# Performance work log

Hardware: AMD Instinct MI355X
Metric: run time of the kernel (lower is better)

The kernel has to match this reference:

```python
import jax, jax.numpy as jnp
import numpy as np
import math

DIM = 32
CODEBOOK_SIZE = 16384
LOG_N = int(math.log(CODEBOOK_SIZE, 2))  # 14
LOGVAR_MIN, LOGVAR_MAX = -30.0, 20.0
TOL = 0.5
BETA = 1.0
LAM = 1.0
LAM_MIN = 1.0
LAM_MAX = 1.0
HALF_LOG_2PI = 0.5 * math.log(2.0 * math.pi)


def setup_inputs() -> dict:
    key = jax.random.key(0)
    k1, k2, k3 = jax.random.split(key, 3)
    z = jax.random.normal(k1, (4, 512, 512), dtype=jnp.float32)
    noise = jax.random.normal(k2, (2048, 256), dtype=jnp.float32)
    # prior_samples buffer: standard-normal codebook [K, DIM]
    codebook = jax.random.normal(k3, (CODEBOOK_SIZE, DIM), dtype=jnp.float32)
    return {"z": z, "noise": noise, "codebook": codebook}


def _forward(z, noise, codebook):
    z_shape = z.shape
    zf = z.reshape(-1, z_shape[-1])                       # [N_tok, 2*DIM*cb]
    cb_num = zf.shape[-1] // (2 * DIM)                    # codebook_num
    mu, logvar = jnp.split(zf, 2, axis=-1)                # each [N_tok, DIM*cb]
    logvar = jnp.clip(logvar, LOGVAR_MIN, LOGVAR_MAX)
    std = jnp.exp(0.5 * logvar)
    var = jnp.exp(logvar)

    # ---- quant_gaussian ----
    zhat_g = mu + noise * std                             # reparam sample
    kl2 = 1.4426 * 0.5 * (mu * mu + var - 1.0 - logvar)
    kl2 = kl2.reshape(-1, DIM, cb_num).sum(axis=1)        # [N_tok, cb]
    ge = (kl2 > LOG_N + TOL).astype(kl2.dtype) * LAM_MAX
    eq = ((kl2 <= LOG_N + TOL) & (kl2 >= LOG_N - TOL)).astype(kl2.dtype)
    le = (kl2 < LOG_N - TOL).astype(kl2.dtype) * LAM_MIN
    kl_loss = jnp.mean(ge * kl2 + eq * kl2 + le * kl2) * LAM

    # ---- quant_vq (Gaussian log-likelihood-ratio codebook search) ----
    # rows: (token, codebook_num) pairs, each with a DIM-dim Gaussian
    mu_r = mu.reshape(-1, DIM, cb_num).transpose(0, 2, 1).reshape(-1, DIM)    # [N, DIM]
    std_r = std.reshape(-1, DIM, cb_num).transpose(0, 2, 1).reshape(-1, DIM)  # [N, DIM]
    inv_var = 1.0 / (std_r * std_r)                                           # [N, DIM]

    c = codebook                                          # [K, DIM]
    c2 = c * c
    # sum_d Normal(mu, std).log_prob(c) expanded into GEMMs over DIM:
    #   -sum log std - DIM/2*log(2pi) - 0.5*(c^2 - 2 c mu + mu^2) / var
    termA = -jnp.sum(jnp.log(std_r), axis=-1) - DIM * HALF_LOG_2PI            # [N]
    quad = 0.5 * (jnp.einsum('nd,kd->nk', inv_var, c2)
                  - 2.0 * jnp.einsum('nd,kd->nk', mu_r * inv_var, c)
                  + jnp.sum(mu_r * mu_r * inv_var, axis=-1, keepdims=True))   # [N, K]
    prior_lp = jnp.sum(-0.5 * c2 - HALF_LOG_2PI, axis=-1)                     # [K]
    perturbed = termA[:, None] - quad - BETA * prior_lp[None, :]              # [N, K]

    indices = jnp.argmax(perturbed, axis=1)               # [N]
    zhat_v = c[indices]                                   # [N, DIM]

    zhat_v = zhat_v.reshape(-1, cb_num, DIM).transpose(0, 2, 1).reshape(-1, cb_num * DIM)
    zhat_v = zhat_v.reshape(*z_shape[:-1], -1)            # [..., DIM*cb]
    zhat_g = zhat_g.reshape(*z_shape[:-1], -1)
    indices = indices.reshape(*z_shape[:-1], cb_num)

    # straight-through estimator (use_ste=True); vq branch is no_grad in torch
    zhat = zhat_g - jax.lax.stop_gradient(zhat_g) + jax.lax.stop_gradient(zhat_v)
    return zhat, kl_loss, indices


def reference(z, noise, codebook):
    return _forward(z, noise, codebook)
```

## Files before the change

### kernel.cpp

```cpp
#include <hip/hip_runtime.h>
#include <math.h>


typedef _Float16 half8 __attribute__((ext_vector_type(8)));
typedef float f32x4 __attribute__((ext_vector_type(4)));

#define DIM 32
#define NROWS 16384
#define KSIZE 16384
#define NSPLIT 16
#define SPLITK 1024
#define NCOL 256

#define WS_M1   0
#define WS_KL   256
#define WS_CN1  512
#define WS_CN2  1536
#define WS_PQ   4096
#define WS_AH   (WS_PQ + 4194304)
#define WS_BH   (WS_AH + 2097152)
#define WS_W1   (WS_BH + 2097152)

__global__ __launch_bounds__(256) void prep_kernel(const float* __restrict__ cb,
                                                   const float* __restrict__ z,
                                                   _Float16* __restrict__ Bh,
                                                   float* __restrict__ CN1,
                                                   float* __restrict__ CN2,
                                                   float* __restrict__ PQ,
                                                   _Float16* __restrict__ Ah,
                                                   double* __restrict__ klsum) {
  const int w = threadIdx.x >> 6, l = threadIdx.x & 63;
  if (blockIdx.x < 512) {
    const int k = blockIdx.x * 32 + w * 8 + (l >> 3);
    const int s_phys = l & 7;
    const int logical = s_phys ^ (k & 7);
    const int base = (logical & 3) * 8;
    const float4 cA = *(const float4*)(cb + k * DIM + base);
    const float4 cB = *(const float4*)(cb + k * DIM + base + 4);
    float v[8] = {cA.x, cA.y, cA.z, cA.w, cB.x, cB.y, cB.z, cB.w};

    half8 hv;
    if (logical < 4) {
#pragma unroll
      for (int i = 0; i < 8; ++i) hv[i] = (_Float16)v[i];
    } else {
#pragma unroll
      for (int i = 0; i < 8; ++i) hv[i] = (_Float16)(v[i] * v[i]);
    }
    *(half8*)(Bh + (size_t)k * 64 + s_phys * 8) = hv;

    float s2 = 0.0f, s4 = 0.0f;
    if (logical < 4) {
#pragma unroll
      for (int i = 0; i < 8; ++i) {
        const float c2 = v[i] * v[i];
        s2 += c2;
        s4 += c2 * c2;
      }
    }
#pragma unroll
    for (int mask = 1; mask <= 4; mask <<= 1) {
      s2 += __shfl_xor(s2, mask);
      s4 += __shfl_xor(s4, mask);
    }
    if (s_phys == 0) {
      const int col = (k >> 10) * 16 + (k & 15);
      atomicMax((unsigned*)&CN1[col], __float_as_uint(sqrtf(s2)));
      atomicMax((unsigned*)&CN2[col], __float_as_uint(sqrtf(s4)));
    }
  } else {
    const int tok = (blockIdx.x - 512) * 4 + w;
    const float4 mu4 = ((const float4*)z)[(size_t)tok * 128 + l];
    const float4 lv4 = ((const float4*)z)[(size_t)tok * 128 + 64 + l];
    const int d = l >> 1;
    const int c0 = (l & 1) * 4;
    double kacc = 0.0;
#pragma unroll
    for (int e = 0; e < 4; ++e) {
      const float mu = ((const float*)&mu4)[e];
      float lv = ((const float*)&lv4)[e];
      lv = fminf(fmaxf(lv, -30.0f), 20.0f);
      const float stdv = expf(0.5f * lv);
      const float iv = 1.0f / (stdv * stdv);
      const float p = mu * iv;
      const float q = 0.5f * (1.0f - iv);
      const size_t row = (size_t)tok * 8 + c0 + e;
      PQ[row * 64 + d] = p;
      PQ[row * 64 + 32 + d] = q;
      Ah[row * 64 + d] = (_Float16)p;
      Ah[row * 64 + 32 + d] = (_Float16)q;
      kacc += (double)(mu * mu + stdv * stdv - 1.0f - lv);
    }
#pragma unroll
    for (int off = 32; off > 0; off >>= 1) kacc += __shfl_down(kacc, off);
    __shared__ double wsum[4];
    if (l == 0) wsum[w] = kacc;
    __syncthreads();
    if (threadIdx.x == 0)
      atomicAdd(klsum, (wsum[0] + wsum[1]) + (wsum[2] + wsum[3]));
  }
}

__device__ __forceinline__ void gload_lds16(const _Float16* g, _Float16* l) {
  __builtin_amdgcn_global_load_lds(
      (__attribute__((address_space(1))) void*)(g),
      (__attribute__((address_space(3))) void*)(l), 16, 0, 0);
}

__global__ __launch_bounds__(256, 2) void filter_kernel(const _Float16* __restrict__ Ah,
                                                        const _Float16* __restrict__ Bh,
                                                        _Float16* __restrict__ W1) {
  __shared__ _Float16 sB[2][16384];
  const int tid = threadIdx.x;
  const int lane = tid & 63;
  const int wave = tid >> 6;
  const int split = blockIdx.y;
  const int rowbase = blockIdx.x * 512 + wave * 128;
  const int c16 = lane & 15, quad = lane >> 4;

  const _Float16* gB = Bh + (size_t)split * SPLITK * 64;

#pragma unroll
  for (int j = 0; j < 8; ++j)
    gload_lds16(gB + j * 2048 + tid * 8, &sB[0][j * 2048 + tid * 8]);

  half8 uh0[8], uh1[8];
#pragma unroll
  for (int rt = 0; rt < 8; ++rt) {
    const size_t abase = (size_t)(rowbase + rt * 16 + c16) * 64 + quad * 8;
    uh0[rt] = *(const half8*)(Ah + abase);
    uh1[rt] = *(const half8*)(Ah + abase + 32);
  }

  float a1[8][4];
#pragma unroll
  for (int rt = 0; rt < 8; ++rt)
#pragma unroll
    for (int r = 0; r < 4; ++r) a1[rt][r] = -INFINITY;

  const f32x4 fzero = {0.f, 0.f, 0.f, 0.f};
  const int key = c16 & 7;
  const int rs0h = c16 * 64 + (quad ^ key) * 8;
  const int rs1h = c16 * 64 + ((quad + 4) ^ key) * 8;

  __syncthreads();

#pragma unroll 1
  for (int ch = 0; ch < 4; ++ch) {
    if (ch < 3) {
      const _Float16* src = gB + (size_t)(ch + 1) * 16384;
      _Float16* dst = &sB[(ch + 1) & 1][0];
#pragma unroll
      for (int j = 0; j < 8; ++j)
        gload_lds16(src + j * 2048 + tid * 8, dst + j * 2048 + tid * 8);
    }
    const _Float16* buf = &sB[ch & 1][0];
#pragma unroll 1
    for (int tp = 0; tp < 8; ++tp) {
      const _Float16* b0 = buf + (2 * tp) * 1024;
      const _Float16* b1 = b0 + 1024;
      const half8 x0 = *(const half8*)(b0 + rs0h);
      const half8 x1 = *(const half8*)(b0 + rs1h);
      const half8 y0 = *(const half8*)(b1 + rs0h);
      const half8 y1 = *(const half8*)(b1 + rs1h);
#pragma unroll
      for (int rt = 0; rt < 8; ++rt) {
        f32x4 h0 = __builtin_amdgcn_mfma_f32_16x16x32_f16(uh0[rt], x0, fzero, 0, 0, 0);
        h0 = __builtin_amdgcn_mfma_f32_16x16x32_f16(uh1[rt], x1, h0, 0, 0, 0);
        f32x4 h1 = __builtin_amdgcn_mfma_f32_16x16x32_f16(uh0[rt], y0, fzero, 0, 0, 0);
        h1 = __builtin_amdgcn_mfma_f32_16x16x32_f16(uh1[rt], y1, h1, 0, 0, 0);
#pragma unroll
        for (int r = 0; r < 4; ++r)
          a1[rt][r] = fmaxf(fmaxf(h0[r], h1[r]), a1[rt][r]);
      }
    }
    __syncthreads();
  }

#pragma unroll
  for (int rt = 0; rt < 8; ++rt)
#pragma unroll
    for (int r = 0; r < 4; ++r) {
      const int row_r = rowbase + rt * 16 + quad * 4 + r;
      W1[((size_t)split * NROWS + row_r) * 16 + c16] =
          (_Float16)fmaxf(a1[rt][r], -65504.0f);
    }
}

__device__ __forceinline__ float exact_score(const float4* __restrict__ cb4,
                                             const float4* __restrict__ spq,
                                             int k) {
  float s0 = 0.0f, s1 = 0.0f, s2 = 0.0f, s3 = 0.0f;
#pragma unroll
  for (int m = 0; m < 8; ++m) {
    const float4 cv = cb4[k * 8 + m];
    const float4 pv = spq[m];
    const float4 qv = spq[8 + m];
    s0 = fmaf(cv.x, fmaf(qv.x, cv.x, pv.x), s0);
    s1 = fmaf(cv.y, fmaf(qv.y, cv.y, pv.y), s1);
    s2 = fmaf(cv.z, fmaf(qv.z, cv.z, pv.z), s2);
    s3 = fmaf(cv.w, fmaf(qv.w, cv.w, pv.w), s3);
  }
  return (s0 + s1) + (s2 + s3);
}

__global__ __launch_bounds__(256, 4) void merge_kernel(const float* __restrict__ PQ,
                                                       const float* __restrict__ cb,
                                                       const _Float16* __restrict__ W1,
                                                       const float* __restrict__ CN1,
                                                       const float* __restrict__ CN2,
                                                       const double* __restrict__ klsum,
                                                       float* __restrict__ out0,
                                                       float* __restrict__ out1,
                                                       float* __restrict__ out2) {
  __shared__ float4 spq_s[4][16];
  const int lane = threadIdx.x & 63;
  const int wave = threadIdx.x >> 6;
  const int row = blockIdx.x * 4 + wave;

  if (lane < 16)
    spq_s[wave][lane] = ((const float4*)(PQ + (size_t)row * 64))[lane];
  __syncthreads();
  const float4* spq = spq_s[wave];
  const float4* __restrict__ cb4 = (const float4*)cb;

  float sp = 0.0f, sq = 0.0f;
  if (lane < DIM) {
    const float pd = ((const float*)spq)[lane];
    const float qd = ((const float*)spq)[32 + lane];
    sp = pd * pd;
    sq = qd * qd;
  }
#pragma unroll
  for (int off = 1; off < 32; off <<= 1) {
    sp += __shfl_xor(sp, off);
    sq += __shfl_xor(sq, off);
  }
  const float pn = sqrtf(__shfl(sp, 0));
  const float qn = sqrtf(__shfl(sq, 0));

  float w[4];
#pragma unroll
  for (int i = 0; i < 4; ++i)
    w[i] = (float)W1[((size_t)(i * 4 + (lane >> 4)) * NROWS + row) * 16 + (lane & 15)];
  float As = fmaxf(fmaxf(w[0], w[1]), fmaxf(w[2], w[3]));
#pragma unroll
  for (int off = 1; off < 64; off <<= 1) As = fmaxf(As, __shfl_xor(As, off));
  const float slack = 2e-5f * (fabsf(As) + 1.0f) + 1e-3f;

  float bt[4];
#pragma unroll
  for (int i = 0; i < 4; ++i) {
    const int col = i * 64 + lane;
    bt[i] = 1.05e-3f * (pn * CN1[col] + qn * CN2[col]) + slack
            + 5e-4f * fabsf(w[i]);
  }

  int done_col = -1;
#pragma unroll
  for (int i = 0; i < 4; ++i) {
    if (done_col < 0) {
      const unsigned long long m = __ballot(w[i] == As);
      if (m) done_col = i * 64 + __builtin_ctzll(m);
    }
  }
  const int k0 = (done_col >> 4) * SPLITK + lane * 16 + (done_col & 15);
  float best = exact_score(cb4, spq, k0);
  int bk = k0;
#pragma unroll
  for (int off = 1; off < 64; off <<= 1) {
    const float ov = __shfl_xor(best, off);
    const int ok = __shfl_xor(bk, off);
    if (ov > best || (ov == best && ok < bk)) { best = ov; bk = ok; }
  }
  const float Estar = best;

#pragma unroll 1
  for (int i = 0; i < 4; ++i) {
    unsigned long long m = __ballot(w[i] + bt[i] >= Estar);
    if ((done_col >> 6) == i) m &= ~(1ull << (done_col & 63));
    while (m) {
      const int e = __builtin_ctzll(m);
      m &= m - 1;
      const int col = i * 64 + e;
      const int k = (col >> 4) * SPLITK + lane * 16 + (col & 15);
      const float sc = exact_score(cb4, spq, k);
      if (sc > best || (sc == best && k < bk)) { best = sc; bk = k; }
    }
  }
#pragma unroll
  for (int off = 1; off < 64; off <<= 1) {
    const float ov = __shfl_xor(best, off);
    const int ok = __shfl_xor(bk, off);
    if (ov > best || (ov == best && ok < bk)) { best = ov; bk = ok; }
  }
  if (lane == 0) out2[row] = (float)bk;
  const int tt = row >> 3, cc = row & 7;
  if (lane < DIM) out0[tt * 256 + lane * 8 + cc] = cb[bk * DIM + lane];
  if (blockIdx.x == 0 && threadIdx.x == 0)
    out1[0] = (float)(klsum[0] * (1.4426 * 0.5) / (double)NROWS);
}

extern "C" void kernel_launch(void* const* d_in, const int* in_sizes, int n_in,
                              void* d_out, int out_size, void* d_ws, size_t ws_size,
                              hipStream_t stream) {
  const float* z  = (const float*)d_in[0];
  const float* cb = (const float*)d_in[2];

  char* ws = (char*)d_ws;
  double* klsum  = (double*)(ws + WS_KL);
  float*     CN1 = (float*)(ws + WS_CN1);
  float*     CN2 = (float*)(ws + WS_CN2);
  float*      PQ = (float*)(ws + WS_PQ);
  _Float16*   Ah = (_Float16*)(ws + WS_AH);
  _Float16*   Bh = (_Float16*)(ws + WS_BH);
  _Float16*   W1 = (_Float16*)(ws + WS_W1);

  float* out0 = (float*)d_out;
  float* out1 = out0 + 524288;
  float* out2 = out1 + 1;

  (void)hipMemsetAsync(ws, 0, 4096, stream);
  prep_kernel<<<1024, 256, 0, stream>>>(cb, z, Bh, CN1, CN2, PQ, Ah, klsum);
  dim3 fgrid(32, NSPLIT);
  filter_kernel<<<fgrid, 256, 0, stream>>>(Ah, Bh, W1);
  merge_kernel<<<NROWS / 4, 256, 0, stream>>>(PQ, cb, W1, CN1, CN2, klsum,
                                              out0, out1, out2);
}
```

Baseline: 128.4 us.

## Process each merge row with a full block and prune candidates by bound threshold

The merge kernel now gives each row a whole 256-thread block instead of one wavefront, with one candidate column per thread. Block reductions go through shared memory. The old exact-score seeding step is replaced by a threshold T, the maximum lower bound (w - bt). Every column whose upper bound reaches T is scored in parallel across the four waves. This spreads the exact rescoring work across more waves, at the cost of four times more blocks, extra barriers, and possibly more candidates because T is looser than the exact best score.

```diff
diff --git a/kernel.cpp b/kernel.cpp
--- a/kernel.cpp
+++ b/kernel.cpp
@@ -213,15 +213,20 @@
                                                        float* __restrict__ out0,
                                                        float* __restrict__ out1,
                                                        float* __restrict__ out2) {
-  __shared__ float4 spq_s[4][16];
-  const int lane = threadIdx.x & 63;
-  const int wave = threadIdx.x >> 6;
-  const int row = blockIdx.x * 4 + wave;
-
-  if (lane < 16)
-    spq_s[wave][lane] = ((const float4*)(PQ + (size_t)row * 64))[lane];
-  __syncthreads();
-  const float4* spq = spq_s[wave];
+  __shared__ float4 spq_s[16];
+  __shared__ float rAs[4], rT[4], rbest[4];
+  __shared__ int rbk[4];
+  const int tid = threadIdx.x;
+  const int lane = tid & 63;
+  const int wave = tid >> 6;
+  const int row = blockIdx.x;
+
+  if (tid < 16)
+    spq_s[tid] = ((const float4*)(PQ + (size_t)row * 64))[tid];
+  const float w = (float)W1[((size_t)(tid >> 4) * NROWS + row) * 16 + (tid & 15)];
+  const float cn1 = CN1[tid], cn2 = CN2[tid];
+  __syncthreads();
+  const float4* spq = spq_s;
   const float4* __restrict__ cb4 = (const float4*)cb;
 
   float sp = 0.0f, sq = 0.0f;
@@ -239,65 +244,54 @@
   const float pn = sqrtf(__shfl(sp, 0));
   const float qn = sqrtf(__shfl(sq, 0));
 
-  float w[4];
-#pragma unroll
-  for (int i = 0; i < 4; ++i)
-    w[i] = (float)W1[((size_t)(i * 4 + (lane >> 4)) * NROWS + row) * 16 + (lane & 15)];
-  float As = fmaxf(fmaxf(w[0], w[1]), fmaxf(w[2], w[3]));
-#pragma unroll
-  for (int off = 1; off < 64; off <<= 1) As = fmaxf(As, __shfl_xor(As, off));
+  float a = w;
+#pragma unroll
+  for (int off = 1; off < 64; off <<= 1) a = fmaxf(a, __shfl_xor(a, off));
+  if (lane == 0) rAs[wave] = a;
+  __syncthreads();
+  const float As = fmaxf(fmaxf(rAs[0], rAs[1]), fmaxf(rAs[2], rAs[3]));
   const float slack = 2e-5f * (fabsf(As) + 1.0f) + 1e-3f;
-
-  float bt[4];
-#pragma unroll
-  for (int i = 0; i < 4; ++i) {
-    const int col = i * 64 + lane;
-    bt[i] = 1.05e-3f * (pn * CN1[col] + qn * CN2[col]) + slack
-            + 5e-4f * fabsf(w[i]);
-  }
-
-  int done_col = -1;
-#pragma unroll
-  for (int i = 0; i < 4; ++i) {
-    if (done_col < 0) {
-      const unsigned long long m = __ballot(w[i] == As);
-      if (m) done_col = i * 64 + __builtin_ctzll(m);
-    }
-  }
-  const int k0 = (done_col >> 4) * SPLITK + lane * 16 + (done_col & 15);
-  float best = exact_score(cb4, spq, k0);
-  int bk = k0;
+  const float bt = 1.05e-3f * (pn * cn1 + qn * cn2) + slack + 5e-4f * fabsf(w);
+
+  float tv = w - bt;
+#pragma unroll
+  for (int off = 1; off < 64; off <<= 1) tv = fmaxf(tv, __shfl_xor(tv, off));
+  if (lane == 0) rT[wave] = tv;
+  __syncthreads();
+  const float T = fmaxf(fmaxf(rT[0], rT[1]), fmaxf(rT[2], rT[3]));
+
+  unsigned long long m = __ballot(w + bt >= T);
+  float best = -INFINITY;
+  int bk = 0x7FFFFFFF;
+  while (m) {
+    const int e = __builtin_ctzll(m);
+    m &= m - 1;
+    const int col = wave * 64 + e;
+    const int k = (col >> 4) * SPLITK + lane * 16 + (col & 15);
+    const float sc = exact_score(cb4, spq, k);
+    if (sc > best || (sc == best && k < bk)) { best = sc; bk = k; }
+  }
 #pragma unroll
   for (int off = 1; off < 64; off <<= 1) {
     const float ov = __shfl_xor(best, off);
     const int ok = __shfl_xor(bk, off);
     if (ov > best || (ov == best && ok < bk)) { best = ov; bk = ok; }
   }
-  const float Estar = best;
-
-#pragma unroll 1
-  for (int i = 0; i < 4; ++i) {
-    unsigned long long m = __ballot(w[i] + bt[i] >= Estar);
-    if ((done_col >> 6) == i) m &= ~(1ull << (done_col & 63));
-    while (m) {
-      const int e = __builtin_ctzll(m);
-      m &= m - 1;
-      const int col = i * 64 + e;
-      const int k = (col >> 4) * SPLITK + lane * 16 + (col & 15);
-      const float sc = exact_score(cb4, spq, k);
-      if (sc > best || (sc == best && k < bk)) { best = sc; bk = k; }
-    }
-  }
-#pragma unroll
-  for (int off = 1; off < 64; off <<= 1) {
-    const float ov = __shfl_xor(best, off);
-    const int ok = __shfl_xor(bk, off);
-    if (ov > best || (ov == best && ok < bk)) { best = ov; bk = ok; }
-  }
-  if (lane == 0) out2[row] = (float)bk;
+  if (lane == 0) { rbest[wave] = best; rbk[wave] = bk; }
+  __syncthreads();
+  float gb = rbest[0];
+  int gk = rbk[0];
+#pragma unroll
+  for (int i = 1; i < 4; ++i) {
+    if (rbest[i] > gb || (rbest[i] == gb && rbk[i] < gk)) {
+      gb = rbest[i];
+      gk = rbk[i];
+    }
+  }
+  if (tid == 0) out2[row] = (float)gk;
   const int tt = row >> 3, cc = row & 7;
-  if (lane < DIM) out0[tt * 256 + lane * 8 + cc] = cb[bk * DIM + lane];
-  if (blockIdx.x == 0 && threadIdx.x == 0)
+  if (tid < DIM) out0[tt * 256 + tid * 8 + cc] = cb[gk * DIM + tid];
+  if (row == 0 && tid == 0)
     out1[0] = (float)(klsum[0] * (1.4426 * 0.5) / (double)NROWS);
 }
 
@@ -324,6 +318,6 @@
   prep_kernel<<<1024, 256, 0, stream>>>(cb, z, Bh, CN1, CN2, PQ, Ah, klsum);
   dim3 fgrid(32, NSPLIT);
   filter_kernel<<<fgrid, 256, 0, stream>>>(Ah, Bh, W1);
-  merge_kernel<<<NROWS / 4, 256, 0, stream>>>(PQ, cb, W1, CN1, CN2, klsum,
-                                              out0, out1, out2);
-}
+  merge_kernel<<<NROWS, 256, 0, stream>>>(PQ, cb, W1, CN1, CN2, klsum,
+                                          out0, out1, out2);
+}
```

New measurement: 163.2 us. 27.1% more time.
